# Performance work log

Measured on AMD Instinct MI355X. Metric: run time of the kernel, lower is better.

Reference implementation:

```python
import jax, jax.numpy as jnp
import numpy as np

B, C, H, W = 16, 128, 64, 64
L, ND = 512, 256
GROUPS = 32
EPS = 1e-6


def setup_inputs() -> dict:
    key = jax.random.key(0)
    ks = jax.random.split(key, 8)
    return {
        "x": jax.random.normal(ks[0], (B, C, H, W), dtype=jnp.float32),
        "nd": jax.random.normal(ks[1], (B, L, ND), dtype=jnp.float32),
        "gn_gamma": jnp.ones((C,), dtype=jnp.float32),
        "gn_beta": jnp.zeros((C,), dtype=jnp.float32),
        "q_w": jax.random.normal(ks[2], (C, C), dtype=jnp.float32) * 0.02,
        "q_b": jax.random.normal(ks[3], (C,), dtype=jnp.float32) * 0.02,
        "nd_w": jax.random.normal(ks[4], (C, ND), dtype=jnp.float32) * 0.02,
        "nd_b": jax.random.normal(ks[5], (C,), dtype=jnp.float32) * 0.02,
        "proj_w": jax.random.normal(ks[6], (C, C), dtype=jnp.float32) * 0.02,
        "proj_b": jax.random.normal(ks[7], (C,), dtype=jnp.float32) * 0.02,
    }


def _group_norm(x, gamma, beta):
    b, c, h, w = x.shape
    xr = x.reshape(b, GROUPS, c // GROUPS, h, w)
    mean = xr.mean(axis=(2, 3, 4), keepdims=True)
    var = xr.var(axis=(2, 3, 4), keepdims=True)
    xn = ((xr - mean) * jax.lax.rsqrt(var + EPS)).reshape(b, c, h, w)
    return xn * gamma[None, :, None, None] + beta[None, :, None, None]


def reference(x, nd, gn_gamma, gn_beta, q_w, q_b, nd_w, nd_b, proj_w, proj_b):
    b, c, h, w = x.shape
    hn = _group_norm(x, gn_gamma, gn_beta)
    # 1x1 conv query -> [b, hw, c]
    q = jnp.einsum('bchw,oc->bhwo', hn, q_w).reshape(b, h * w, c) + q_b
    # silu + linear projection of conditioning; k and v use identical projection/input
    kv = jax.nn.silu(nd) @ nd_w.T + nd_b  # [b, L, c]
    # attention: [b, hw, L]
    logits = jnp.einsum('bnc,blc->bnl', q, kv) * (c ** -0.5)
    attn = jax.nn.softmax(logits, axis=2)
    # weighted sum of v -> [b, c, hw] -> [b, c, h, w]
    out = jnp.einsum('blc,bnl->bcn', kv, attn).reshape(b, c, h, w)
    # 1x1 conv projection
    out = jnp.einsum('bchw,oc->bohw', out, proj_w) + proj_b[None, :, None, None]
    return x + out
```

## Files before the change

kernel.cpp:

```cpp
#include <hip/hip_runtime.h>
#include <math.h>

constexpr int kB = 16, kC = 128, kHW = 4096, kL = 512, kND = 256, kG = 32;
constexpr float kEps = 1e-6f;
constexpr float kScale = 0.08838834764831845f;

typedef short sv8 __attribute__((ext_vector_type(8)));
typedef int   iv4 __attribute__((ext_vector_type(4)));
typedef float f32x16 __attribute__((ext_vector_type(16)));

static __device__ __forceinline__ unsigned short f2bf(float f) {
    unsigned int u = __builtin_bit_cast(unsigned int, f);
    u += 0x7fffu + ((u >> 16) & 1u);
    return (unsigned short)(u >> 16);
}
static __device__ __forceinline__ float bf2f(unsigned short s) {
    unsigned int u = ((unsigned int)s) << 16;
    return __builtin_bit_cast(float, u);
}
static __device__ __forceinline__ unsigned int pack2(float a, float b) {
    return (unsigned int)f2bf(a) | ((unsigned int)f2bf(b) << 16);
}

#define GLOAD_LDS16(gp, lp)                                                     \
    __builtin_amdgcn_global_load_lds(                                           \
        (const __attribute__((address_space(1))) void*)(gp),                    \
        (__attribute__((address_space(3))) void*)(lp), 16, 0, 0)

__global__ __launch_bounds__(256) void prep_all_k(
    const float* __restrict__ x, const float* __restrict__ nd,
    const float* __restrict__ nd_w, const float* __restrict__ nd_b,
    const float* __restrict__ proj_w, const float* __restrict__ q_w,
    float* __restrict__ stats, unsigned short* __restrict__ kv_bf,
    unsigned short* __restrict__ kvT_bf, unsigned short* __restrict__ pwb,
    unsigned short* __restrict__ qwb)
{
    __shared__ float s_lds[8][256];
    __shared__ float w_lds[128][68];
    __shared__ float t_lds[8][129];
    __shared__ float red8[8];
    const int bid = blockIdx.x;
    const int tid = threadIdx.x;

    if (bid < 512) {
        const float4* p4 = (const float4*)(x + (size_t)bid * 4 * kHW);
        float s = 0.f, ss = 0.f;
        for (int i = tid; i < 4096; i += 256) {
            float4 v = p4[i];
            s  += (v.x + v.y) + (v.z + v.w);
            ss += (v.x * v.x + v.y * v.y) + (v.z * v.z + v.w * v.w);
        }
#pragma unroll
        for (int off = 1; off < 64; off <<= 1) {
            s  += __shfl_xor(s, off, 64);
            ss += __shfl_xor(ss, off, 64);
        }
        int wid = tid >> 6;
        if ((tid & 63) == 0) { red8[wid] = s; red8[wid + 4] = ss; }
        __syncthreads();
        if (tid == 0) {
            float S  = (red8[0] + red8[1]) + (red8[2] + red8[3]);
            float SS = (red8[4] + red8[5]) + (red8[6] + red8[7]);
            float mean = S * (1.f / 16384.f);
            float var  = SS * (1.f / 16384.f) - mean * mean;
            stats[bid * 2]     = mean;
            stats[bid * 2 + 1] = rsqrtf(var + kEps);
        }
        return;
    }
    if (bid >= 1536) {
        const float* src = (bid < 1552) ? proj_w : q_w;
        unsigned short* dst = (bid < 1552) ? pwb : qwb;
        int i = (((bid - 1536) & 15) * 256 + tid) * 4;
        float4 v = *(const float4*)(src + i);
        dst[i + 0] = f2bf(v.x); dst[i + 1] = f2bf(v.y);
        dst[i + 2] = f2bf(v.z); dst[i + 3] = f2bf(v.w);
        return;
    }
    {
        int idx0 = bid - 512;
        int b = idx0 >> 6;
        int l0 = (idx0 & 63) * 8;
        const float4* ndp = (const float4*)(nd + ((size_t)b * kL + l0) * kND);
#pragma unroll
        for (int r = 0; r < 2; r++) {
            int idx = tid + r * 256;
            int row = idx >> 6;
            int c4 = idx & 63;
            float4 v = ndp[row * 64 + c4];
            v.x = v.x / (1.f + __expf(-v.x));
            v.y = v.y / (1.f + __expf(-v.y));
            v.z = v.z / (1.f + __expf(-v.z));
            v.w = v.w / (1.f + __expf(-v.w));
            *(float4*)&s_lds[row][c4 * 4] = v;
        }
        float acc[4] = {0.f, 0.f, 0.f, 0.f};
        int lr = tid >> 5;
        int oq = tid & 31;
        for (int d0 = 0; d0 < kND; d0 += 64) {
            __syncthreads();
#pragma unroll
            for (int r = 0; r < 8; r++) {
                int idx = tid + r * 256;
                int row = idx >> 4;
                int c4 = idx & 15;
                float4 v = ((const float4*)(nd_w + (size_t)row * kND + d0))[c4];
                *(float4*)&w_lds[row][c4 * 4] = v;
            }
            __syncthreads();
            for (int dd = 0; dd < 64; dd += 4) {
                float4 sv = *(const float4*)&s_lds[lr][d0 + dd];
#pragma unroll
                for (int j = 0; j < 4; j++) {
                    float4 wv = *(const float4*)&w_lds[oq + 32 * j][dd];
                    acc[j] += sv.x * wv.x + sv.y * wv.y + sv.z * wv.z + sv.w * wv.w;
                }
            }
        }
#pragma unroll
        for (int j = 0; j < 4; j++) {
            int o = oq + 32 * j;
            float vout = acc[j] + nd_b[o];
            kv_bf[((size_t)b * kL + l0 + lr) * kC + o] = f2bf(vout);
            t_lds[lr][o] = vout;
        }
        __syncthreads();
        int o = tid >> 1, lh = (tid & 1) * 4;
        unsigned long long pk = 0;
#pragma unroll
        for (int i = 0; i < 4; i++)
            pk |= (unsigned long long)f2bf(t_lds[lh + i][o]) << (16 * i);
        *(unsigned long long*)(kvT_bf + ((size_t)b * kC + o) * kL + l0 + lh) = pk;
    }
}

__global__ __launch_bounds__(128, 4) void qproj_k(
    const float* __restrict__ x, const float* __restrict__ stats,
    const float* __restrict__ gamma, const float* __restrict__ beta,
    const unsigned short* __restrict__ qwb, const float* __restrict__ q_b,
    unsigned short* __restrict__ q_bf)
{
    __shared__ __align__(16) char smem[8704];
    float* hn_f = (float*)smem;
    unsigned short* q_out = (unsigned short*)smem;

    const int b = blockIdx.y;
    const int n0 = blockIdx.x * 32;
    const int tid = threadIdx.x;
    const int wave = tid >> 6;
    const int lane = tid & 63;
    const int lrow = lane & 31;
    const int hi = lane >> 5;

    f32x16 dq[2];
#pragma unroll
    for (int ot = 0; ot < 2; ot++)
#pragma unroll
        for (int r = 0; r < 16; r++) dq[ot][r] = 0.f;

    for (int cc = 0; cc < 4; cc++) {
#pragma unroll
        for (int k = 0; k < 2; k++) {
            int idx = tid + k * 128;
            int cl = idx >> 3, n4 = idx & 7;
            int c = cc * 32 + cl;
            float4 v = *(const float4*)(
                x + ((size_t)b * kC + c) * kHW + n0 + n4 * 4);
            float mean = stats[(b * kG + (c >> 2)) * 2];
            float rstd = stats[(b * kG + (c >> 2)) * 2 + 1];
            float ga = gamma[c] * rstd;
            float be = beta[c] - mean * ga;
            v.x = v.x * ga + be; v.y = v.y * ga + be;
            v.z = v.z * ga + be; v.w = v.w * ga + be;
            *(float4*)&hn_f[cl * 32 + n4 * 4] = v;
        }
        __syncthreads();
        sv8 bh[2];
#pragma unroll
        for (int kk = 0; kk < 2; kk++) {
            sv8 a;
#pragma unroll
            for (int j = 0; j < 8; j++)
                a[j] = (short)f2bf(hn_f[(kk * 16 + hi * 8 + j) * 32 + lrow]);
            bh[kk] = a;
        }
#pragma unroll
        for (int ot = 0; ot < 2; ot++) {
            const unsigned short* arow =
                qwb + (size_t)(wave * 64 + ot * 32 + lrow) * kC + cc * 32 + hi * 8;
#pragma unroll
            for (int kk = 0; kk < 2; kk++)
                dq[ot] = __builtin_amdgcn_mfma_f32_32x32x16_bf16(
                             *(const sv8*)(arow + kk * 16), bh[kk], dq[ot], 0, 0, 0);
        }
        __syncthreads();
    }
#pragma unroll
    for (int ot = 0; ot < 2; ot++) {
#pragma unroll
        for (int g = 0; g < 4; g++) {
            int ob = wave * 64 + ot * 32 + 8 * g + 4 * hi;
            float4 qb4 = *(const float4*)(q_b + ob);
            q_out[lrow * 136 + ob + 0] = f2bf((dq[ot][4 * g + 0] + qb4.x) * kScale);
            q_out[lrow * 136 + ob + 1] = f2bf((dq[ot][4 * g + 1] + qb4.y) * kScale);
            q_out[lrow * 136 + ob + 2] = f2bf((dq[ot][4 * g + 2] + qb4.z) * kScale);
            q_out[lrow * 136 + ob + 3] = f2bf((dq[ot][4 * g + 3] + qb4.w) * kScale);
        }
    }
    __syncthreads();
#pragma unroll
    for (int r = 0; r < 4; r++) {
        int idx = tid + r * 128;
        int n = idx >> 4, ch = idx & 15;
        *(uint4*)(q_bf + ((size_t)b * kHW + n0 + n) * kC + ch * 8) =
            *(const uint4*)&q_out[n * 136 + ch * 8];
    }
}

__global__ __launch_bounds__(256, 2) void attn_k(
    const unsigned short* __restrict__ qb,
    const unsigned short* __restrict__ kvb,
    const unsigned short* __restrict__ kvtb,
    const unsigned short* __restrict__ pwb,
    const float* __restrict__ proj_b,
    const float* __restrict__ x,
    float* __restrict__ out)
{
    __shared__ __align__(16) char smem[35328];

    const int flat = blockIdx.y * gridDim.x + blockIdx.x;
    const int b  = ((flat & 7) << 1) | ((flat >> 3) & 1);
    const int n0 = (flat >> 4) * 128;
    const int tid = threadIdx.x;
    const int wave = tid >> 6;
    const int lane = tid & 63;
    const int lrow = lane & 31;
    const int hi = lane >> 5;
    const int swzA = (lrow & 15) << 4;
    const int swzT = ((lrow >> 1) & 3) << 4;

    sv8 qa[8];
    {
        const unsigned short* qrow =
            qb + ((size_t)b * kHW + n0 + wave * 32 + lrow) * kC + hi * 8;
#pragma unroll
        for (int kc = 0; kc < 8; kc++)
            qa[kc] = *(const sv8*)(qrow + kc * 16);
    }

    f32x16 oacc[4];
#pragma unroll
    for (int ct = 0; ct < 4; ct++)
#pragma unroll
        for (int r = 0; r < 16; r++) oacc[ct][r] = 0.f;
    float rsumv = 0.f;

    const unsigned short* kvB  = kvb  + (size_t)b * kL * kC;
    const unsigned short* kvtB = kvtb + (size_t)b * kC * kL;

#define STAGE_TILE(tt) do {                                                     \
        int l0s = (tt) << 5;                                                    \
        char* dA = smem + (((tt) & 1) * 8192);                                  \
        char* dT = smem + 16384 + (((tt) & 1) * 8192);                          \
        _Pragma("unroll")                                                       \
        for (int i = 0; i < 2; i++) {                                           \
            int l = i * 16 + wave * 4 + (lane >> 4);                            \
            int ch = lane & 15;                                                 \
            const unsigned short* gs =                                          \
                kvB + (size_t)(l0s + l) * kC + ((ch ^ (l & 15)) * 8);           \
            GLOAD_LDS16(gs, dA + (i * 256 + wave * 64) * 16);                   \
        }                                                                       \
        _Pragma("unroll")                                                       \
        for (int i = 0; i < 2; i++) {                                           \
            int c = i * 64 + wave * 16 + (lane >> 2);                           \
            int ch = lane & 3;                                                  \
            const unsigned short* gs =                                          \
                kvtB + (size_t)c * kL + l0s + ((ch ^ ((c >> 1) & 3)) * 8);      \
            GLOAD_LDS16(gs, dT + (i * 256 + wave * 64) * 16);                   \
        }                                                                       \
    } while (0)

    STAGE_TILE(0);
    __syncthreads();

    for (int t = 0; t < 16; t++) {
        const char* bufA = smem + (t & 1) * 8192;
        const char* bufT = smem + 16384 + (t & 1) * 8192;
        if (t < 15) STAGE_TILE(t + 1);

        f32x16 s;
#pragma unroll
        for (int r = 0; r < 16; r++) s[r] = 0.f;
        {
            const char* arow = bufA + lrow * 256;
            __builtin_amdgcn_s_setprio(1);
#pragma unroll
            for (int kc = 0; kc < 8; kc++)
                s = __builtin_amdgcn_mfma_f32_32x32x16_bf16(
                        *(const sv8*)(arow + ((kc * 32 + hi * 16) ^ swzA)),
                        qa[kc], s, 0, 0, 0);
            __builtin_amdgcn_s_setprio(0);
        }
        float p[16];
#pragma unroll
        for (int r = 0; r < 16; r++) {
            p[r] = __expf(s[r]);
            rsumv += p[r];
        }
        unsigned int pk[4], pk2[4];
#pragma unroll
        for (int g = 0; g < 4; g++) {
            pk[g]  = pack2(p[4 * g + 0], p[4 * g + 1]);
            pk2[g] = pack2(p[4 * g + 2], p[4 * g + 3]);
        }
        sv8 pv[2];
#pragma unroll
        for (int kk = 0; kk < 2; kk++) {
            unsigned int a_lo = pk[kk * 2],  a_hi = pk[kk * 2 + 1];
            unsigned int b_lo = pk2[kk * 2], b_hi = pk2[kk * 2 + 1];
            unsigned int own_a = hi ? a_hi : a_lo;
            unsigned int own_b = hi ? b_hi : b_lo;
            unsigned int rcv_a = (unsigned int)__shfl_xor((int)(hi ? a_lo : a_hi), 32, 64);
            unsigned int rcv_b = (unsigned int)__shfl_xor((int)(hi ? b_lo : b_hi), 32, 64);
            iv4 w;
            w[0] = (int)(hi ? rcv_a : own_a);
            w[1] = (int)(hi ? rcv_b : own_b);
            w[2] = (int)(hi ? own_a : rcv_a);
            w[3] = (int)(hi ? own_b : rcv_b);
            pv[kk] = __builtin_bit_cast(sv8, w);
        }
        __builtin_amdgcn_s_setprio(1);
#pragma unroll
        for (int ct = 0; ct < 4; ct++) {
            const char* rowp = bufT + (ct * 32 + lrow) * 64;
#pragma unroll
            for (int kk = 0; kk < 2; kk++)
                oacc[ct] = __builtin_amdgcn_mfma_f32_32x32x16_bf16(
                               pv[kk],
                               *(const sv8*)(rowp + ((kk * 32 + hi * 16) ^ swzT)),
                               oacc[ct], 0, 0, 0);
        }
        __builtin_amdgcn_s_setprio(0);

        __syncthreads();
    }

    float total = rsumv + __shfl_xor(rsumv, 32, 64);
    float* rs = (float*)(smem + 34816) + wave * 32;
    rs[lrow] = 1.0f / total;
    float rinv[16];
#pragma unroll
    for (int r = 0; r < 16; r++)
        rinv[r] = rs[(r & 3) + 8 * (r >> 2) + 4 * hi];

    unsigned short* o_lds = (unsigned short*)smem;
    __syncthreads();
#pragma unroll
    for (int ct = 0; ct < 4; ct++)
#pragma unroll
        for (int r = 0; r < 16; r++) {
            int n = wave * 32 + (r & 3) + 8 * (r >> 2) + 4 * hi;
            o_lds[n * 136 + ct * 32 + lrow] = f2bf(oacc[ct][r] * rinv[r]);
        }
    sv8 oa[8];
    {
        const unsigned short* orow = o_lds + (wave * 32 + lrow) * 136 + hi * 8;
#pragma unroll
        for (int kc = 0; kc < 8; kc++) oa[kc] = *(const sv8*)(orow + kc * 16);
    }
    f32x16 dacc[4];
#pragma unroll
    for (int ot = 0; ot < 4; ot++)
#pragma unroll
        for (int r = 0; r < 16; r++) dacc[ot][r] = 0.f;
#pragma unroll
    for (int ot = 0; ot < 4; ot++) {
        const unsigned short* brow = pwb + (ot * 32 + lrow) * kC + hi * 8;
#pragma unroll
        for (int kc = 0; kc < 8; kc++)
            dacc[ot] = __builtin_amdgcn_mfma_f32_32x32x16_bf16(
                           oa[kc], *(const sv8*)(brow + kc * 16), dacc[ot], 0, 0, 0);
    }
#pragma unroll
    for (int ot = 0; ot < 4; ot++)
#pragma unroll
        for (int r = 0; r < 16; r++) {
            int n = wave * 32 + (r & 3) + 8 * (r >> 2) + 4 * hi;
            o_lds[n * 136 + ot * 32 + lrow] = f2bf(dacc[ot][r]);
        }
    __syncthreads();
#pragma unroll 4
    for (int it = 0; it < 64; it++) {
        int idx = it * 256 + tid;
        int o = idx >> 7, n = idx & 127;
        size_t gi = ((size_t)b * kC + o) * kHW + n0 + n;
        out[gi] = bf2f(o_lds[n * 136 + o]) + proj_b[o] + x[gi];
    }
#undef STAGE_TILE
}

extern "C" void kernel_launch(void* const* d_in, const int* in_sizes, int n_in,
                              void* d_out, int out_size, void* d_ws, size_t ws_size,
                              hipStream_t stream) {
    const float* x      = (const float*)d_in[0];
    const float* nd     = (const float*)d_in[1];
    const float* gamma  = (const float*)d_in[2];
    const float* beta   = (const float*)d_in[3];
    const float* q_w    = (const float*)d_in[4];
    const float* q_b    = (const float*)d_in[5];
    const float* nd_w   = (const float*)d_in[6];
    const float* nd_b   = (const float*)d_in[7];
    const float* proj_w = (const float*)d_in[8];
    const float* proj_b = (const float*)d_in[9];
    float* out = (float*)d_out;

    float* stats           = (float*)d_ws;
    unsigned short* pwb    = (unsigned short*)(stats + 1024);
    unsigned short* qwb    = pwb + 16384;
    unsigned short* kv_bf  = qwb + 16384;
    unsigned short* kvT_bf = kv_bf + (size_t)kB * kL * kC;
    unsigned short* q_bf   = kvT_bf + (size_t)kB * kL * kC;

    prep_all_k<<<dim3(1568), dim3(256), 0, stream>>>(
        x, nd, nd_w, nd_b, proj_w, q_w, stats, kv_bf, kvT_bf, pwb, qwb);
    qproj_k<<<dim3(kHW / 32, kB), dim3(128), 0, stream>>>(
        x, stats, gamma, beta, qwb, q_b, q_bf);
    attn_k<<<dim3(kHW / 128, kB), dim3(256), 0, stream>>>(
        q_bf, kv_bf, kvT_bf, pwb, proj_b, x, out);
}
```

Measured before the change: 93.99 us.

## Stage two KV tiles per barrier and precompute GroupNorm scale/shift

```diff
diff --git a/kernel.cpp b/kernel.cpp
--- a/kernel.cpp
+++ b/kernel.cpp
@@ -31,7 +31,8 @@
     const float* __restrict__ x, const float* __restrict__ nd,
     const float* __restrict__ nd_w, const float* __restrict__ nd_b,
     const float* __restrict__ proj_w, const float* __restrict__ q_w,
-    float* __restrict__ stats, unsigned short* __restrict__ kv_bf,
+    const float* __restrict__ gamma, const float* __restrict__ beta,
+    float* __restrict__ gab, unsigned short* __restrict__ kv_bf,
     unsigned short* __restrict__ kvT_bf, unsigned short* __restrict__ pwb,
     unsigned short* __restrict__ qwb)
 {
@@ -63,8 +64,16 @@
             float SS = (red8[4] + red8[5]) + (red8[6] + red8[7]);
             float mean = S * (1.f / 16384.f);
             float var  = SS * (1.f / 16384.f) - mean * mean;
-            stats[bid * 2]     = mean;
-            stats[bid * 2 + 1] = rsqrtf(var + kEps);
+            red8[0] = mean;
+            red8[1] = rsqrtf(var + kEps);
+        }
+        __syncthreads();
+        if (tid < 4) {
+            int bb = bid >> 5, g = bid & 31, c = g * 4 + tid;
+            float mean = red8[0], rstd = red8[1];
+            float ga = gamma[c] * rstd;
+            gab[(bb * 128 + c) * 2]     = ga;
+            gab[(bb * 128 + c) * 2 + 1] = beta[c] - mean * ga;
         }
         return;
     }
@@ -135,14 +144,14 @@
 }
 
 __global__ __launch_bounds__(128, 4) void qproj_k(
-    const float* __restrict__ x, const float* __restrict__ stats,
-    const float* __restrict__ gamma, const float* __restrict__ beta,
+    const float* __restrict__ x, const float* __restrict__ gab,
     const unsigned short* __restrict__ qwb, const float* __restrict__ q_b,
     unsigned short* __restrict__ q_bf)
 {
-    __shared__ __align__(16) char smem[8704];
+    __shared__ __align__(16) char smem[9728];
     float* hn_f = (float*)smem;
     unsigned short* q_out = (unsigned short*)smem;
+    float* gtab = (float*)(smem + 8704);
 
     const int b = blockIdx.y;
     const int n0 = blockIdx.x * 32;
@@ -152,6 +161,10 @@
     const int lrow = lane & 31;
     const int hi = lane >> 5;
 
+    if (tid < 64)
+        *(float4*)&gtab[tid * 4] = ((const float4*)(gab + b * 256))[tid];
+    __syncthreads();
+
     f32x16 dq[2];
 #pragma unroll
     for (int ot = 0; ot < 2; ot++)
@@ -166,10 +179,7 @@
             int c = cc * 32 + cl;
             float4 v = *(const float4*)(
                 x + ((size_t)b * kC + c) * kHW + n0 + n4 * 4);
-            float mean = stats[(b * kG + (c >> 2)) * 2];
-            float rstd = stats[(b * kG + (c >> 2)) * 2 + 1];
-            float ga = gamma[c] * rstd;
-            float be = beta[c] - mean * ga;
+            float ga = gtab[c * 2], be = gtab[c * 2 + 1];
             v.x = v.x * ga + be; v.y = v.y * ga + be;
             v.z = v.z * ga + be; v.w = v.w * ga + be;
             *(float4*)&hn_f[cl * 32 + n4 * 4] = v;
@@ -226,7 +236,7 @@
     const float* __restrict__ x,
     float* __restrict__ out)
 {
-    __shared__ __align__(16) char smem[35328];
+    __shared__ __align__(16) char smem[66048];
 
     const int flat = blockIdx.y * gridDim.x + blockIdx.x;
     const int b  = ((flat & 7) << 1) | ((flat >> 3) & 1);
@@ -258,95 +268,106 @@
     const unsigned short* kvB  = kvb  + (size_t)b * kL * kC;
     const unsigned short* kvtB = kvtb + (size_t)b * kC * kL;
 
-#define STAGE_TILE(tt) do {                                                     \
-        int l0s = (tt) << 5;                                                    \
-        char* dA = smem + (((tt) & 1) * 8192);                                  \
-        char* dT = smem + 16384 + (((tt) & 1) * 8192);                          \
-        _Pragma("unroll")                                                       \
-        for (int i = 0; i < 2; i++) {                                           \
-            int l = i * 16 + wave * 4 + (lane >> 4);                            \
-            int ch = lane & 15;                                                 \
-            const unsigned short* gs =                                          \
-                kvB + (size_t)(l0s + l) * kC + ((ch ^ (l & 15)) * 8);           \
-            GLOAD_LDS16(gs, dA + (i * 256 + wave * 64) * 16);                   \
+    int offA[2], offT[2], dst[2];
+#pragma unroll
+    for (int i = 0; i < 2; i++) {
+        int l = i * 16 + wave * 4 + (lane >> 4);
+        offA[i] = l * kC + (((lane & 15) ^ (l & 15)) * 8);
+        int c = i * 64 + wave * 16 + (lane >> 2);
+        offT[i] = c * kL + (((lane & 3) ^ ((c >> 1) & 3)) * 8);
+        dst[i] = (i * 256 + wave * 64) * 16;
+    }
+
+#define STAGE1(tt, slot) do {                                                   \
+        const unsigned short* _sA = kvB + (size_t)(tt) * (32 * kC);             \
+        const unsigned short* _sT = kvtB + (tt) * 32;                           \
+        char* _dA = smem + (slot) * 8192;                                       \
+        char* _dT = smem + 32768 + (slot) * 8192;                               \
+        _Pragma("unroll")                                                       \
+        for (int i = 0; i < 2; i++) GLOAD_LDS16(_sA + offA[i], _dA + dst[i]);   \
+        _Pragma("unroll")                                                       \
+        for (int i = 0; i < 2; i++) GLOAD_LDS16(_sT + offT[i], _dT + dst[i]);   \
+    } while (0)
+
+#define COMPUTE1(slot) do {                                                     \
+        const char* bufA = smem + (slot) * 8192;                                \
+        const char* bufT = smem + 32768 + (slot) * 8192;                        \
+        f32x16 s0, s1;                                                          \
+        _Pragma("unroll")                                                       \
+        for (int r = 0; r < 16; r++) { s0[r] = 0.f; s1[r] = 0.f; }              \
+        const char* arow = bufA + lrow * 256;                                   \
+        __builtin_amdgcn_s_setprio(1);                                          \
+        _Pragma("unroll")                                                       \
+        for (int kc = 0; kc < 4; kc++) {                                        \
+            s0 = __builtin_amdgcn_mfma_f32_32x32x16_bf16(                       \
+                     *(const sv8*)(arow + ((kc * 32 + hi * 16) ^ swzA)),        \
+                     qa[kc], s0, 0, 0, 0);                                      \
+            s1 = __builtin_amdgcn_mfma_f32_32x32x16_bf16(                       \
+                     *(const sv8*)(arow + (((kc + 4) * 32 + hi * 16) ^ swzA)),  \
+                     qa[kc + 4], s1, 0, 0, 0);                                  \
         }                                                                       \
-        _Pragma("unroll")                                                       \
-        for (int i = 0; i < 2; i++) {                                           \
-            int c = i * 64 + wave * 16 + (lane >> 2);                           \
-            int ch = lane & 3;                                                  \
-            const unsigned short* gs =                                          \
-                kvtB + (size_t)c * kL + l0s + ((ch ^ ((c >> 1) & 3)) * 8);      \
-            GLOAD_LDS16(gs, dT + (i * 256 + wave * 64) * 16);                   \
+        __builtin_amdgcn_s_setprio(0);                                          \
+        float p[16];                                                            \
+        _Pragma("unroll")                                                       \
+        for (int r = 0; r < 16; r++) {                                          \
+            p[r] = __expf(s0[r] + s1[r]);                                       \
+            rsumv += p[r];                                                      \
         }                                                                       \
+        unsigned int pk[4], pk2[4];                                             \
+        _Pragma("unroll")                                                       \
+        for (int g = 0; g < 4; g++) {                                           \
+            pk[g]  = pack2(p[4 * g + 0], p[4 * g + 1]);                         \
+            pk2[g] = pack2(p[4 * g + 2], p[4 * g + 3]);                         \
+        }                                                                       \
+        sv8 pv[2];                                                              \
+        _Pragma("unroll")                                                       \
+        for (int kk = 0; kk < 2; kk++) {                                        \
+            unsigned int a_lo = pk[kk * 2],  a_hi = pk[kk * 2 + 1];             \
+            unsigned int b_lo = pk2[kk * 2], b_hi = pk2[kk * 2 + 1];            \
+            unsigned int own_a = hi ? a_hi : a_lo;                              \
+            unsigned int own_b = hi ? b_hi : b_lo;                              \
+            unsigned int rcv_a =                                                \
+                (unsigned int)__shfl_xor((int)(hi ? a_lo : a_hi), 32, 64);      \
+            unsigned int rcv_b =                                                \
+                (unsigned int)__shfl_xor((int)(hi ? b_lo : b_hi), 32, 64);      \
+            iv4 w;                                                              \
+            w[0] = (int)(hi ? rcv_a : own_a);                                   \
+            w[1] = (int)(hi ? rcv_b : own_b);                                   \
+            w[2] = (int)(hi ? own_a : rcv_a);                                   \
+            w[3] = (int)(hi ? own_b : rcv_b);                                   \
+            pv[kk] = __builtin_bit_cast(sv8, w);                                \
+        }                                                                       \
+        __builtin_amdgcn_s_setprio(1);                                          \
+        _Pragma("unroll")                                                       \
+        for (int ct = 0; ct < 4; ct++) {                                        \
+            const char* rowp = bufT + (ct * 32 + lrow) * 64;                    \
+            _Pragma("unroll")                                                   \
+            for (int kk = 0; kk < 2; kk++)                                      \
+                oacc[ct] = __builtin_amdgcn_mfma_f32_32x32x16_bf16(             \
+                               pv[kk],                                          \
+                               *(const sv8*)(rowp + ((kk * 32 + hi * 16) ^ swzT)), \
+                               oacc[ct], 0, 0, 0);                              \
+        }                                                                       \
+        __builtin_amdgcn_s_setprio(0);                                          \
     } while (0)
 
-    STAGE_TILE(0);
+    STAGE1(0, 0);
+    STAGE1(1, 1);
     __syncthreads();
 
-    for (int t = 0; t < 16; t++) {
-        const char* bufA = smem + (t & 1) * 8192;
-        const char* bufT = smem + 16384 + (t & 1) * 8192;
-        if (t < 15) STAGE_TILE(t + 1);
-
-        f32x16 s;
-#pragma unroll
-        for (int r = 0; r < 16; r++) s[r] = 0.f;
-        {
-            const char* arow = bufA + lrow * 256;
-            __builtin_amdgcn_s_setprio(1);
-#pragma unroll
-            for (int kc = 0; kc < 8; kc++)
-                s = __builtin_amdgcn_mfma_f32_32x32x16_bf16(
-                        *(const sv8*)(arow + ((kc * 32 + hi * 16) ^ swzA)),
-                        qa[kc], s, 0, 0, 0);
-            __builtin_amdgcn_s_setprio(0);
-        }
-        float p[16];
-#pragma unroll
-        for (int r = 0; r < 16; r++) {
-            p[r] = __expf(s[r]);
-            rsumv += p[r];
-        }
-        unsigned int pk[4], pk2[4];
-#pragma unroll
-        for (int g = 0; g < 4; g++) {
-            pk[g]  = pack2(p[4 * g + 0], p[4 * g + 1]);
-            pk2[g] = pack2(p[4 * g + 2], p[4 * g + 3]);
-        }
-        sv8 pv[2];
-#pragma unroll
-        for (int kk = 0; kk < 2; kk++) {
-            unsigned int a_lo = pk[kk * 2],  a_hi = pk[kk * 2 + 1];
-            unsigned int b_lo = pk2[kk * 2], b_hi = pk2[kk * 2 + 1];
-            unsigned int own_a = hi ? a_hi : a_lo;
-            unsigned int own_b = hi ? b_hi : b_lo;
-            unsigned int rcv_a = (unsigned int)__shfl_xor((int)(hi ? a_lo : a_hi), 32, 64);
-            unsigned int rcv_b = (unsigned int)__shfl_xor((int)(hi ? b_lo : b_hi), 32, 64);
-            iv4 w;
-            w[0] = (int)(hi ? rcv_a : own_a);
-            w[1] = (int)(hi ? rcv_b : own_b);
-            w[2] = (int)(hi ? own_a : rcv_a);
-            w[3] = (int)(hi ? own_b : rcv_b);
-            pv[kk] = __builtin_bit_cast(sv8, w);
-        }
-        __builtin_amdgcn_s_setprio(1);
-#pragma unroll
-        for (int ct = 0; ct < 4; ct++) {
-            const char* rowp = bufT + (ct * 32 + lrow) * 64;
-#pragma unroll
-            for (int kk = 0; kk < 2; kk++)
-                oacc[ct] = __builtin_amdgcn_mfma_f32_32x32x16_bf16(
-                               pv[kk],
-                               *(const sv8*)(rowp + ((kk * 32 + hi * 16) ^ swzT)),
-                               oacc[ct], 0, 0, 0);
-        }
-        __builtin_amdgcn_s_setprio(0);
-
+    for (int it = 0; it < 8; it++) {
+        int pr = it & 1;
+        if (it < 7) {
+            STAGE1(2 * it + 2, 2 * (pr ^ 1));
+            STAGE1(2 * it + 3, 2 * (pr ^ 1) + 1);
+        }
+        COMPUTE1(2 * pr);
+        COMPUTE1(2 * pr + 1);
         __syncthreads();
     }
 
     float total = rsumv + __shfl_xor(rsumv, 32, 64);
-    float* rs = (float*)(smem + 34816) + wave * 32;
+    float* rs = (float*)(smem + 65536) + wave * 32;
     rs[lrow] = 1.0f / total;
     float rinv[16];
 #pragma unroll
@@ -396,7 +417,8 @@
         size_t gi = ((size_t)b * kC + o) * kHW + n0 + n;
         out[gi] = bf2f(o_lds[n * 136 + o]) + proj_b[o] + x[gi];
     }
-#undef STAGE_TILE
+#undef STAGE1
+#undef COMPUTE1
 }
 
 extern "C" void kernel_launch(void* const* d_in, const int* in_sizes, int n_in,
@@ -414,17 +436,17 @@
     const float* proj_b = (const float*)d_in[9];
     float* out = (float*)d_out;
 
-    float* stats           = (float*)d_ws;
-    unsigned short* pwb    = (unsigned short*)(stats + 1024);
+    float* gab             = (float*)d_ws;
+    unsigned short* pwb    = (unsigned short*)(gab + 4096);
     unsigned short* qwb    = pwb + 16384;
     unsigned short* kv_bf  = qwb + 16384;
     unsigned short* kvT_bf = kv_bf + (size_t)kB * kL * kC;
     unsigned short* q_bf   = kvT_bf + (size_t)kB * kL * kC;
 
     prep_all_k<<<dim3(1568), dim3(256), 0, stream>>>(
-        x, nd, nd_w, nd_b, proj_w, q_w, stats, kv_bf, kvT_bf, pwb, qwb);
+        x, nd, nd_w, nd_b, proj_w, q_w, gamma, beta, gab, kv_bf, kvT_bf, pwb, qwb);
     qproj_k<<<dim3(kHW / 32, kB), dim3(128), 0, stream>>>(
-        x, stats, gamma, beta, qwb, q_b, q_bf);
+        x, gab, qwb, q_b, q_bf);
     attn_k<<<dim3(kHW / 128, kB), dim3(256), 0, stream>>>(
         q_bf, kv_bf, kvT_bf, pwb, proj_b, x, out);
 }
```

Result: faster. 90.02 us (-4.2%).
